# Optimization experiments

Hardware: AMD Instinct MI355X
Metric: run time of the kernel (lower is better)

## Reference

```python
import jax, jax.numpy as jnp
import numpy as np

E, B, C_IN, H, W = 4, 32, 64, 64, 64
C_OUT, KH, KW = 128, 3, 3


def setup_inputs() -> dict:
    key = jax.random.key(0)
    k1, k2 = jax.random.split(key)
    features = jax.random.normal(k1, (E, B, C_IN, H, W), dtype=jnp.float32)
    # weight: ensemble + (in, out) + kernel, Glorot-style std = out_channels**-0.5
    weight = jax.random.normal(k2, (E, C_IN, C_OUT, KH, KW), dtype=jnp.float32) * (C_OUT ** -0.5)
    bias = jnp.zeros((E, C_OUT), dtype=jnp.float32)
    return {"features": features, "weight": weight, "bias": bias}


def reference(features, weight, bias):
    # features: (E, B, C_in, H, W); weight: (E, C_in, C_out, KH, KW); bias: (E, C_out)
    # The torch module's unfold+einsum equals a VALID cross-correlation per ensemble member:
    # out[e,b,j,y,x] = sum_{i,A,B} features[e,b,i,y+A,x+B] * weight[e,i,j,A,B]
    def conv_one(x, w):
        k = jnp.transpose(w, (1, 0, 2, 3))  # (C_out, C_in, KH, KW) = OIHW
        return jax.lax.conv_general_dilated(
            x, k, window_strides=(1, 1), padding="VALID",
            dimension_numbers=("NCHW", "OIHW", "NCHW"))

    out = jax.vmap(conv_one)(features, weight)  # (E, B, C_out, H', W')
    out = out + bias[:, None, :, None, None]
    return out
```

## Files before the change

### kernel.cpp

```cpp
#include <hip/hip_runtime.h>

typedef __bf16 bf16x8 __attribute__((ext_vector_type(8)));
typedef __bf16 bf16x2 __attribute__((ext_vector_type(2)));
typedef float  f32x4  __attribute__((ext_vector_type(4)));

#define FT_BYTES 67108864ull

__device__ __forceinline__ void gl2lds16(const void* g, void* l) {
    __builtin_amdgcn_global_load_lds(
        (const __attribute__((address_space(1))) void*)g,
        (__attribute__((address_space(3))) void*)l, 16, 0, 0);
}

__global__ void wt_prep(const float* __restrict__ w, __bf16* __restrict__ wt) {
    int o = blockIdx.x * 256 + threadIdx.x;
    int i = o & 63, j = (o >> 6) & 127, et = o >> 13;
    int tap = et % 9, e = et / 9;
    wt[o] = (__bf16)w[((e * 64 + i) * 128 + j) * 9 + tap];
}

__global__ void ft_prep(const float* __restrict__ f, __bf16* __restrict__ ft) {
    __shared__ float s[64 * 65];
    int eb = blockIdx.z * 32 + blockIdx.y, y = blockIdx.x;
    const float* src = f + (size_t)eb * 262144 + y * 64;
    int t = threadIdx.x;
    for (int r = 0; r < 4; ++r) {
        int f4 = r * 256 + t;
        int i = f4 >> 4, x4 = (f4 & 15) * 4;
        float4 v = *(const float4*)(src + i * 4096 + x4);
        s[i * 65 + x4 + 0] = v.x; s[i * 65 + x4 + 1] = v.y;
        s[i * 65 + x4 + 2] = v.z; s[i * 65 + x4 + 3] = v.w;
    }
    __syncthreads();
    bf16x2* dst = (bf16x2*)(ft + (size_t)(eb * 64 + y) * 4096);
    for (int r = 0; r < 8; ++r) {
        int q = r * 256 + t;
        int x = q >> 5, ih = q & 31;
        bf16x2 pv;
        pv.x = (__bf16)s[(2 * ih + 0) * 65 + x];
        pv.y = (__bf16)s[(2 * ih + 1) * 65 + x];
        dst[q] = pv;
    }
}

__global__ __launch_bounds__(512, 2)
void conv_main(const __bf16* __restrict__ ft, const __bf16* __restrict__ wt,
               const float* __restrict__ bias, float* __restrict__ out) {
    __shared__ __align__(16) __bf16 sW[9 * 4096];
    __shared__ __align__(16) __bf16 sF[2][16384];
    const int y0 = blockIdx.x * 2, jh = blockIdx.y;
    const int e = blockIdx.z >> 1, bg = blockIdx.z & 1;
    const int t = threadIdx.x, lane = t & 63, w = t >> 6;
    const int wm = w >> 2, wn = w & 3;
    const int q = lane >> 4, rm = lane & 15;

    const __bf16* wte = wt + ((size_t)(e * 9) << 13) + (jh << 12);
    for (int k = 0; k < 9; ++k) {
        int s = w * 9 + k;
        int tap = s >> 3;
        int r = (s & 7) * 8 + (lane >> 3);
        int g = (lane & 7) ^ (r & 7);
        gl2lds16(wte + (tap << 13) + r * 64 + g * 8, sW + s * 512);
    }
    const __bf16* fte = ft + ((size_t)(e * 32 + bg * 16) << 18) + ((size_t)y0 << 12);
    for (int cc = 0; cc < 4; ++cc) {
        int c = w * 4 + cc;
        int r = c * 8 + (lane >> 3);
        int g = (lane & 7) ^ (r & 7);
        gl2lds16(fte + (r << 6) + g * 8, sF[0] + c * 512);
    }

    float bias_r[2][4];
    for (int mi = 0; mi < 2; ++mi)
        for (int vv = 0; vv < 4; ++vv)
            bias_r[mi][vv] = bias[e * 128 + jh * 64 + wm * 32 + mi * 16 + q * 4 + vv];

    __syncthreads();

    #pragma unroll 1
    for (int it = 0; it < 16; ++it) {
        const int buf = it & 1;
        const __bf16* sFb = sF[buf];
        if (it < 15) {
            const __bf16* fn = fte + (((size_t)(it + 1)) << 18);
            for (int cc = 0; cc < 4; ++cc) {
                int c = w * 4 + cc;
                int r = c * 8 + (lane >> 3);
                int g = (lane & 7) ^ (r & 7);
                gl2lds16(fn + (r << 6) + g * 8, sF[buf ^ 1] + c * 512);
            }
        }

        f32x4 acc[2][2] = {};
        #pragma unroll
        for (int tap = 0; tap < 9; ++tap) {
            const int A = tap / 3, Bt = tap - A * 3;
            const __bf16* sWt = sW + tap * 4096;
            #pragma unroll
            for (int kh = 0; kh < 2; ++kh) {
                const int kg = kh * 4;
                bf16x8 af[2], bq[2];
                #pragma unroll
                for (int mi = 0; mi < 2; ++mi) {
                    int r = wm * 32 + mi * 16 + rm;
                    int ch = (kg + q) ^ (r & 7);
                    af[mi] = *(const bf16x8*)(sWt + r * 64 + ch * 8);
                }
                #pragma unroll
                for (int ni = 0; ni < 2; ++ni) {
                    int p = wn * 32 + ni * 16 + rm;
                    int py = p >> 6, px = p & 63;
                    int xx = px + Bt; if (xx > 63) xx = 63;
                    int r2 = (A + py) * 64 + xx;
                    int ch = (kg + q) ^ (r2 & 7);
                    bq[ni] = *(const bf16x8*)(sFb + r2 * 64 + ch * 8);
                }
                #pragma unroll
                for (int mi = 0; mi < 2; ++mi)
                    #pragma unroll
                    for (int ni = 0; ni < 2; ++ni)
                        acc[mi][ni] = __builtin_amdgcn_mfma_f32_16x16x32_bf16(
                            af[mi], bq[ni], acc[mi][ni], 0, 0, 0);
            }
        }

        const size_t eb = (size_t)(e * 32 + bg * 16 + it);
        for (int mi = 0; mi < 2; ++mi) {
            for (int ni = 0; ni < 2; ++ni) {
                int p = wn * 32 + ni * 16 + rm;
                int py = p >> 6, px = p & 63;
                if (px >= 62) continue;
                for (int vv = 0; vv < 4; ++vv) {
                    int j = jh * 64 + wm * 32 + mi * 16 + q * 4 + vv;
                    float v = acc[mi][ni][vv] + bias_r[mi][vv];
                    out[((eb * 128 + j) * 62 + (y0 + py)) * 62 + px] = v;
                }
            }
        }
        if (it < 15) __syncthreads();
    }
}

extern "C" void kernel_launch(void* const* d_in, const int* in_sizes, int n_in,
                              void* d_out, int out_size, void* d_ws, size_t ws_size,
                              hipStream_t stream) {
    const float* f    = (const float*)d_in[0];
    const float* wgt  = (const float*)d_in[1];
    const float* bias = (const float*)d_in[2];
    float* out = (float*)d_out;
    __bf16* ftw = (__bf16*)d_ws;
    __bf16* wtw = (__bf16*)((char*)d_ws + FT_BYTES);

    ft_prep<<<dim3(64, 32, 4), 256, 0, stream>>>(f, ftw);
    wt_prep<<<dim3(1152), 256, 0, stream>>>(wgt, wtw);
    conv_main<<<dim3(31, 2, 8), 512, 0, stream>>>(ftw, wtw, bias, out);
}
```

Before: 424.1 us.

## Keep conv weights in registers and compute all output channels per block

After: 449.8 us. +6.1%, slower.

```diff
diff --git a/kernel.cpp b/kernel.cpp
--- a/kernel.cpp
+++ b/kernel.cpp
@@ -46,23 +46,26 @@
 __global__ __launch_bounds__(512, 2)
 void conv_main(const __bf16* __restrict__ ft, const __bf16* __restrict__ wt,
                const float* __restrict__ bias, float* __restrict__ out) {
-    __shared__ __align__(16) __bf16 sW[9 * 4096];
     __shared__ __align__(16) __bf16 sF[2][16384];
-    const int y0 = blockIdx.x * 2, jh = blockIdx.y;
-    const int e = blockIdx.z >> 1, bg = blockIdx.z & 1;
+    const int y0 = blockIdx.x * 2, bg = blockIdx.y, e = blockIdx.z;
     const int t = threadIdx.x, lane = t & 63, w = t >> 6;
-    const int wm = w >> 2, wn = w & 3;
+    const int wm = w >> 1, wn = w & 1;
     const int q = lane >> 4, rm = lane & 15;
 
-    const __bf16* wte = wt + ((size_t)(e * 9) << 13) + (jh << 12);
-    for (int k = 0; k < 9; ++k) {
-        int s = w * 9 + k;
-        int tap = s >> 3;
-        int r = (s & 7) * 8 + (lane >> 3);
-        int g = (lane & 7) ^ (r & 7);
-        gl2lds16(wte + (tap << 13) + r * 64 + g * 8, sW + s * 512);
-    }
-    const __bf16* fte = ft + ((size_t)(e * 32 + bg * 16) << 18) + ((size_t)y0 << 12);
+    const __bf16* wbase = wt + ((size_t)(e * 9) << 13)
+                        + (wm * 32 + rm) * 64 + q * 8;
+    bf16x8 af[2][2][9];
+    #pragma unroll
+    for (int tap = 0; tap < 9; ++tap)
+        #pragma unroll
+        for (int mi = 0; mi < 2; ++mi)
+            #pragma unroll
+            for (int kh = 0; kh < 2; ++kh)
+                af[mi][kh][tap] =
+                    *(const bf16x8*)(wbase + tap * 8192 + mi * 1024 + kh * 32);
+
+    const __bf16* fte = ft + ((size_t)(e * 32 + bg * 16) << 18)
+                      + ((size_t)y0 << 12);
     for (int cc = 0; cc < 4; ++cc) {
         int c = w * 4 + cc;
         int r = c * 8 + (lane >> 3);
@@ -71,9 +74,11 @@
     }
 
     float bias_r[2][4];
+    #pragma unroll
     for (int mi = 0; mi < 2; ++mi)
+        #pragma unroll
         for (int vv = 0; vv < 4; ++vv)
-            bias_r[mi][vv] = bias[e * 128 + jh * 64 + wm * 32 + mi * 16 + q * 4 + vv];
+            bias_r[mi][vv] = bias[e * 128 + wm * 32 + mi * 16 + q * 4 + vv];
 
     __syncthreads();
 
@@ -82,7 +87,7 @@
         const int buf = it & 1;
         const __bf16* sFb = sF[buf];
         if (it < 15) {
-            const __bf16* fn = fte + (((size_t)(it + 1)) << 18);
+            const __bf16* fn = fte + ((size_t)(it + 1) << 18);
             for (int cc = 0; cc < 4; ++cc) {
                 int c = w * 4 + cc;
                 int r = c * 8 + (lane >> 3);
@@ -91,24 +96,17 @@
             }
         }
 
-        f32x4 acc[2][2] = {};
+        f32x4 acc[2][4] = {};
         #pragma unroll
         for (int tap = 0; tap < 9; ++tap) {
             const int A = tap / 3, Bt = tap - A * 3;
-            const __bf16* sWt = sW + tap * 4096;
             #pragma unroll
             for (int kh = 0; kh < 2; ++kh) {
                 const int kg = kh * 4;
-                bf16x8 af[2], bq[2];
+                bf16x8 bq[4];
                 #pragma unroll
-                for (int mi = 0; mi < 2; ++mi) {
-                    int r = wm * 32 + mi * 16 + rm;
-                    int ch = (kg + q) ^ (r & 7);
-                    af[mi] = *(const bf16x8*)(sWt + r * 64 + ch * 8);
-                }
-                #pragma unroll
-                for (int ni = 0; ni < 2; ++ni) {
-                    int p = wn * 32 + ni * 16 + rm;
+                for (int ni = 0; ni < 4; ++ni) {
+                    int p = wn * 64 + ni * 16 + rm;
                     int py = p >> 6, px = p & 63;
                     int xx = px + Bt; if (xx > 63) xx = 63;
                     int r2 = (A + py) * 64 + xx;
@@ -118,20 +116,20 @@
                 #pragma unroll
                 for (int mi = 0; mi < 2; ++mi)
                     #pragma unroll
-                    for (int ni = 0; ni < 2; ++ni)
+                    for (int ni = 0; ni < 4; ++ni)
                         acc[mi][ni] = __builtin_amdgcn_mfma_f32_16x16x32_bf16(
-                            af[mi], bq[ni], acc[mi][ni], 0, 0, 0);
+                            af[mi][kh][tap], bq[ni], acc[mi][ni], 0, 0, 0);
             }
         }
 
         const size_t eb = (size_t)(e * 32 + bg * 16 + it);
         for (int mi = 0; mi < 2; ++mi) {
-            for (int ni = 0; ni < 2; ++ni) {
-                int p = wn * 32 + ni * 16 + rm;
+            for (int ni = 0; ni < 4; ++ni) {
+                int p = wn * 64 + ni * 16 + rm;
                 int py = p >> 6, px = p & 63;
                 if (px >= 62) continue;
                 for (int vv = 0; vv < 4; ++vv) {
-                    int j = jh * 64 + wm * 32 + mi * 16 + q * 4 + vv;
+                    int j = wm * 32 + mi * 16 + q * 4 + vv;
                     float v = acc[mi][ni][vv] + bias_r[mi][vv];
                     out[((eb * 128 + j) * 62 + (y0 + py)) * 62 + px] = v;
                 }
@@ -153,5 +151,5 @@
 
     ft_prep<<<dim3(64, 32, 4), 256, 0, stream>>>(f, ftw);
     wt_prep<<<dim3(1152), 256, 0, stream>>>(wgt, wtw);
-    conv_main<<<dim3(31, 2, 8), 512, 0, stream>>>(ftw, wtw, bias, out);
+    conv_main<<<dim3(31, 2, 4), 512, 0, stream>>>(ftw, wtw, bias, out);
 }
```
